# Performance work log

Measured on AMD Instinct MI355X. Metric: run time of the kernel, lower is better.

The kernel has to match this reference:

```python
import jax, jax.numpy as jnp
import numpy as np

BEV_H = 100
BEV_W = 100
BEV_Z = 4
NUM_CAMS = 6
EMBED = 256
HF, WF = 32, 88
PC_RANGE = (-51.2, -51.2, -5.0, 51.2, 51.2, 3.0)
EPS = 1e-5


def setup_inputs() -> dict:
    key = jax.random.key(0)
    ks = jax.random.split(key, 5)
    B, Nq = 1, BEV_H * BEV_W
    return {
        "query": jax.random.normal(ks[0], (B, Nq, EMBED), jnp.float32),
        "img_feats": jax.random.normal(ks[1], (B, NUM_CAMS, EMBED, HF, WF), jnp.float32),
        "lidar2img": jax.random.normal(ks[2], (B, NUM_CAMS, 4, 4), jnp.float32),
        "attn_w": jax.random.normal(ks[3], (EMBED, NUM_CAMS * BEV_Z), jnp.float32) * 0.02,
        "attn_b": jnp.zeros((NUM_CAMS * BEV_Z,), jnp.float32),
        "out_w": jax.random.normal(ks[4], (EMBED, EMBED), jnp.float32) * 0.02,
        "out_b": jnp.zeros((EMBED,), jnp.float32),
    }


def _reference_points(B):
    # normalized pillar reference points: (B, Nq, Z, 3), x,y,z in (0,1)
    ys = jnp.linspace(0.5, BEV_H - 0.5, BEV_H, dtype=jnp.float32) / BEV_H
    xs = jnp.linspace(0.5, BEV_W - 0.5, BEV_W, dtype=jnp.float32) / BEV_W
    ref_y, ref_x = jnp.meshgrid(ys, xs, indexing="ij")  # (H, W)
    Nq = BEV_H * BEV_W
    rx = jnp.broadcast_to(ref_x.reshape(Nq, 1), (Nq, BEV_Z))
    ry = jnp.broadcast_to(ref_y.reshape(Nq, 1), (Nq, BEV_Z))
    rz = jnp.broadcast_to(
        (jnp.linspace(0.5, BEV_Z - 0.5, BEV_Z, dtype=jnp.float32) / BEV_Z)[None, :],
        (Nq, BEV_Z),
    )
    ref = jnp.stack([rx, ry, rz], axis=-1)  # (Nq, Z, 3)
    return jnp.broadcast_to(ref[None], (B, Nq, BEV_Z, 3))


def _grid_sample(img, grid):
    # Bilinear grid_sample, zero padding, align_corners=False.
    # img: (M, C, H, W), grid: (M, N, 2) in [-1, 1] -> (M, C, N)
    M, C, H, W = img.shape
    x = ((grid[..., 0] + 1.0) * W - 1.0) * 0.5
    y = ((grid[..., 1] + 1.0) * H - 1.0) * 0.5
    x0 = jnp.floor(x)
    y0 = jnp.floor(y)
    wx1 = x - x0
    wy1 = y - y0

    def tap(xi, yi, w):
        valid = (xi >= 0) & (xi < W) & (yi >= 0) & (yi < H)
        xc = jnp.clip(xi, 0, W - 1).astype(jnp.int32)
        yc = jnp.clip(yi, 0, H - 1).astype(jnp.int32)
        v = jax.vmap(lambda im, yy, xx: im[:, yy, xx])(img, yc, xc)  # (M, C, N)
        return v * (w * valid)[:, None, :]

    return (
        tap(x0, y0, (1.0 - wx1) * (1.0 - wy1))
        + tap(x0 + 1.0, y0, wx1 * (1.0 - wy1))
        + tap(x0, y0 + 1.0, (1.0 - wx1) * wy1)
        + tap(x0 + 1.0, y0 + 1.0, wx1 * wy1)
    )


def reference(query, img_feats, lidar2img, attn_w, attn_b, out_w, out_b):
    B, Nq, C = query.shape
    Ncam = img_feats.shape[1]
    Hf, Wf = img_feats.shape[-2], img_feats.shape[-1]
    Z = BEV_Z

    ref = _reference_points(B)  # (B, Nq, Z, 3)
    pc = PC_RANGE
    scale = jnp.array([pc[3] - pc[0], pc[4] - pc[1], pc[5] - pc[2]], jnp.float32)
    offset = jnp.array([pc[0], pc[1], pc[2]], jnp.float32)
    r = ref * scale + offset
    r4 = jnp.concatenate([r, jnp.ones_like(r[..., :1])], axis=-1).reshape(B, Nq * Z, 4)

    # project to each camera: (B, Ncam, Nq*Z, 4)
    cam = jnp.einsum("bnij,bqj->bnqi", lidar2img, r4)
    depth = cam[..., 2]
    xy = cam[..., 0:2] / jnp.maximum(depth, EPS)[..., None]
    gx = (xy[..., 0] / (Wf - 1) - 0.5) * 2.0
    gy = (xy[..., 1] / (Hf - 1) - 0.5) * 2.0
    grid = jnp.stack([gx, gy], axis=-1)  # (B, Ncam, Nq*Z, 2)
    valid = (depth > EPS) & (gx > -1.0) & (gx < 1.0) & (gy > -1.0) & (gy < 1.0)

    sampled = _grid_sample(
        img_feats.reshape(B * Ncam, C, Hf, Wf), grid.reshape(B * Ncam, Nq * Z, 2)
    )  # (B*Ncam, C, Nq*Z)
    sampled = sampled.reshape(B, Ncam, C, Nq, Z) * valid.reshape(B, Ncam, 1, Nq, Z)
    sampled = jnp.nan_to_num(sampled)

    # (cam, z) softmax weights from the query
    w = jax.nn.softmax(query @ attn_w + attn_b, axis=-1).reshape(B, Nq, Ncam, Z)
    out = jnp.einsum("bncqz,bqnz->bqc", sampled, w)
    out = out @ out_w + out_b
    return out + query
```

## Files before the change

kernel.cpp:

```cpp
#include <hip/hip_runtime.h>
#include <math.h>

#define NCAM 6
#define CH   256
#define HFt  32
#define WFt  88
#define NQ   10000
#define NPT  24

typedef __attribute__((ext_vector_type(8))) short short8;
typedef __attribute__((ext_vector_type(4))) float f32x4;

__device__ __forceinline__ unsigned short f2bf(float x) {
  unsigned int u = __float_as_uint(x);
  u += 0x7FFFu + ((u >> 16) & 1u);
  return (unsigned short)(u >> 16);
}
__device__ __forceinline__ float bf2f(unsigned short b) {
  return __uint_as_float(((unsigned int)b) << 16);
}

#define TRBLKS  (NCAM * HFt * 8)
#define WSWBLKS 32
#define LOGITS0 (TRBLKS + WSWBLKS)
#define NLB     157

__global__ __launch_bounds__(256) void k_prep(const float* __restrict__ img,
                                              const float* __restrict__ query,
                                              const float* __restrict__ aw,
                                              const float* __restrict__ ab,
                                              const float* __restrict__ ow,
                                              unsigned short* __restrict__ featT,
                                              unsigned short* __restrict__ Wsw,
                                              float* __restrict__ Wgt) {
  __shared__ __align__(16) char smem[16384];
  const int blk = blockIdx.x;
  const int tid = threadIdx.x;

  if (blk < TRBLKS) {
    float (*tile)[WFt + 1] = (float (*)[WFt + 1])smem;
    int ct = blk & 7, h = (blk >> 3) & 31, cam = blk >> 8;
    const float* src = img + (((size_t)cam * CH + ct * 32) * HFt + h) * WFt;
    for (int i = tid; i < 32 * 22; i += 256) {
      int c = i / 22, w4 = i - c * 22;
      float4 v = *(const float4*)(src + (size_t)c * (HFt * WFt) + 4 * w4);
      tile[c][4 * w4 + 0] = v.x;
      tile[c][4 * w4 + 1] = v.y;
      tile[c][4 * w4 + 2] = v.z;
      tile[c][4 * w4 + 3] = v.w;
    }
    __syncthreads();
    unsigned short* dst = featT + ((size_t)(cam * HFt + h) * WFt) * CH + ct * 32;
    for (int i = tid; i < WFt * 8; i += 256) {
      int w = i >> 3, g = i & 7;
      uint2 u;
      u.x = (unsigned int)f2bf(tile[4 * g + 0][w]) | ((unsigned int)f2bf(tile[4 * g + 1][w]) << 16);
      u.y = (unsigned int)f2bf(tile[4 * g + 2][w]) | ((unsigned int)f2bf(tile[4 * g + 3][w]) << 16);
      *(uint2*)(dst + (size_t)w * CH + 4 * g) = u;
    }
    return;
  }

  if (blk < LOGITS0) {
    int gtid = (blk - TRBLKS) * 256 + tid;
    int l  = gtid & 63;
    int f  = (gtid >> 6) & 1;
    int kk = (gtid >> 7) & 7;
    int c  = gtid >> 10;
    int n  = 32 * c + 16 * f + (l & 15);
    int kb = 32 * kk + 4 * (l >> 4);
    unsigned int u0 = f2bf(ow[(kb + 0) * CH + n])  | ((unsigned int)f2bf(ow[(kb + 1) * CH + n])  << 16);
    unsigned int u1 = f2bf(ow[(kb + 2) * CH + n])  | ((unsigned int)f2bf(ow[(kb + 3) * CH + n])  << 16);
    unsigned int u2 = f2bf(ow[(kb + 16) * CH + n]) | ((unsigned int)f2bf(ow[(kb + 17) * CH + n]) << 16);
    unsigned int u3 = f2bf(ow[(kb + 18) * CH + n]) | ((unsigned int)f2bf(ow[(kb + 19) * CH + n]) << 16);
    ((uint4*)Wsw)[gtid] = make_uint4(u0, u1, u2, u3);
    return;
  }

  const int q0 = (blk - LOGITS0) * 64;
  uint4* awB = (uint4*)smem;
  for (int e = tid; e < 1024; e += 256) {
    int le = e & 63, f = (e >> 6) & 1, kk = e >> 7;
    int n = 16 * f + (le & 15);
    int kb = 32 * kk + 4 * (le >> 4);
    uint4 uv = make_uint4(0u, 0u, 0u, 0u);
    if (n < NPT) {
      uv.x = f2bf(aw[(kb + 0) * NPT + n])  | ((unsigned int)f2bf(aw[(kb + 1) * NPT + n])  << 16);
      uv.y = f2bf(aw[(kb + 2) * NPT + n])  | ((unsigned int)f2bf(aw[(kb + 3) * NPT + n])  << 16);
      uv.z = f2bf(aw[(kb + 16) * NPT + n]) | ((unsigned int)f2bf(aw[(kb + 17) * NPT + n]) << 16);
      uv.w = f2bf(aw[(kb + 18) * NPT + n]) | ((unsigned int)f2bf(aw[(kb + 19) * NPT + n]) << 16);
    }
    awB[e] = uv;
  }
  __syncthreads();

  const int wv = tid >> 6, l = tid & 63;
  const int col = l & 15, grp = l >> 4;
  int qr = q0 + wv * 16 + col;
  if (qr > NQ - 1) qr = NQ - 1;
  const float* qp = query + (size_t)qr * CH + 4 * grp;

  f32x4 acc0 = {0.f, 0.f, 0.f, 0.f}, acc1 = {0.f, 0.f, 0.f, 0.f};
#pragma unroll
  for (int kk = 0; kk < 8; kk++) {
    float4 lo = *(const float4*)(qp + kk * 32);
    float4 hi = *(const float4*)(qp + kk * 32 + 16);
    union { uint4 u; short8 s; } a;
    a.u.x = (unsigned int)f2bf(lo.x) | ((unsigned int)f2bf(lo.y) << 16);
    a.u.y = (unsigned int)f2bf(lo.z) | ((unsigned int)f2bf(lo.w) << 16);
    a.u.z = (unsigned int)f2bf(hi.x) | ((unsigned int)f2bf(hi.y) << 16);
    a.u.w = (unsigned int)f2bf(hi.z) | ((unsigned int)f2bf(hi.w) << 16);
    union { uint4 u; short8 s; } b0, b1;
    b0.u = awB[(kk * 2 + 0) * 64 + l];
    b1.u = awB[(kk * 2 + 1) * 64 + l];
    acc0 = __builtin_amdgcn_mfma_f32_16x16x32_bf16(a.s, b0.s, acc0, 0, 0, 0);
    acc1 = __builtin_amdgcn_mfma_f32_16x16x32_bf16(a.s, b1.s, acc1, 0, 0, 0);
  }

  const int n0 = col, n1 = 16 + col;
  const bool v16 = (n1 < NPT);
  const float ab0 = ab[n0];
  const float ab1 = v16 ? ab[n1] : 0.f;
#pragma unroll
  for (int r = 0; r < 4; r++) {
    float v0 = acc0[r] + ab0;
    float v1 = v16 ? (acc1[r] + ab1) : -3.4e38f;
    float m = fmaxf(v0, v1);
#pragma unroll
    for (int off = 1; off < 16; off <<= 1) m = fmaxf(m, __shfl_xor(m, off, 64));
    float e0 = __expf(v0 - m);
    float e1 = v16 ? __expf(v1 - m) : 0.f;
    float s = e0 + e1;
#pragma unroll
    for (int off = 1; off < 16; off <<= 1) s += __shfl_xor(s, off, 64);
    int qq = q0 + wv * 16 + 4 * grp + r;
    if (qq < NQ) {
      Wgt[qq * NPT + n0] = e0 / s;
      if (v16) Wgt[qq * NPT + n1] = e1 / s;
    }
  }
}

__global__ __launch_bounds__(256) void k_main(const unsigned short* __restrict__ featT,
                                              const float* __restrict__ l2i,
                                              const float* __restrict__ Wgt,
                                              unsigned short* __restrict__ A) {
  const int wv   = threadIdx.x >> 6;
  const int lane = threadIdx.x & 63;
  const int q    = blockIdx.x * 4 + wv;

  __shared__ float Lm[NCAM * 16];
  __shared__ int   offW[4][96];
  __shared__ float wW[4][96];

  if (threadIdx.x < NCAM * 16) Lm[threadIdx.x] = l2i[threadIdx.x];

  float sw = (lane < NPT) ? Wgt[q * NPT + lane] : 0.f;

  __syncthreads();

  bool valid = false;
  int o0 = 0, o1 = 0, o2 = 0, o3 = 0;
  float w0 = 0.f, w1 = 0.f, w2 = 0.f, w3 = 0.f;
  if (lane < NPT) {
    int cam = lane >> 2, z = lane & 3;
    float X  = (((q % 100) + 0.5f) * 0.01f) * 102.4f - 51.2f;
    float Y  = (((q / 100) + 0.5f) * 0.01f) * 102.4f - 51.2f;
    float Zc = ((z + 0.5f) * 0.25f) * 8.f - 5.f;
    const float* Lr = Lm + cam * 16;
    float cx = Lr[0] * X + Lr[1] * Y + Lr[2]  * Zc + Lr[3];
    float cy = Lr[4] * X + Lr[5] * Y + Lr[6]  * Zc + Lr[7];
    float cd = Lr[8] * X + Lr[9] * Y + Lr[10] * Zc + Lr[11];
    float d  = fmaxf(cd, 1e-5f);
    float gx = (cx / d * (1.f / 87.f) - 0.5f) * 2.f;
    float gy = (cy / d * (1.f / 31.f) - 0.5f) * 2.f;
    valid = (cd > 1e-5f) && (gx > -1.f) && (gx < 1.f) && (gy > -1.f) && (gy < 1.f);

    float x = ((gx + 1.f) * 88.f - 1.f) * 0.5f;
    float y = ((gy + 1.f) * 32.f - 1.f) * 0.5f;
    float x0f = floorf(x), y0f = floorf(y);
    float wx1 = x - x0f, wy1 = y - y0f;
    float wx0 = 1.f - wx1, wy0 = 1.f - wy1;
    bool vx0 = (x0f >= 0.f) && (x0f < 88.f);
    bool vx1 = (x0f + 1.f >= 0.f) && (x0f + 1.f < 88.f);
    bool vy0 = (y0f >= 0.f) && (y0f < 32.f);
    bool vy1 = (y0f + 1.f >= 0.f) && (y0f + 1.f < 32.f);
    int x0 = (int)fminf(fmaxf(x0f, 0.f), 87.f);
    int x1 = (int)fminf(fmaxf(x0f + 1.f, 0.f), 87.f);
    int y0 = (int)fminf(fmaxf(y0f, 0.f), 31.f);
    int y1 = (int)fminf(fmaxf(y0f + 1.f, 0.f), 31.f);
    int cb = cam * (HFt * WFt);
    o0 = (cb + y0 * WFt + x0) * CH;
    o1 = (cb + y0 * WFt + x1) * CH;
    o2 = (cb + y1 * WFt + x0) * CH;
    o3 = (cb + y1 * WFt + x1) * CH;
    w0 = sw * wx0 * wy0 * ((vx0 && vy0) ? 1.f : 0.f);
    w1 = sw * wx1 * wy0 * ((vx1 && vy0) ? 1.f : 0.f);
    w2 = sw * wx0 * wy1 * ((vx0 && vy1) ? 1.f : 0.f);
    w3 = sw * wx1 * wy1 * ((vx1 && vy1) ? 1.f : 0.f);
  }

  unsigned long long vm = __ballot(valid);
  int nvalid = __popcll(vm);
  int pos = __popcll(vm & ((1ull << lane) - 1ull));
  if (valid) {
    int b = 4 * pos;
    offW[wv][b + 0] = o0; wW[wv][b + 0] = w0;
    offW[wv][b + 1] = o1; wW[wv][b + 1] = w1;
    offW[wv][b + 2] = o2; wW[wv][b + 2] = w2;
    offW[wv][b + 3] = o3; wW[wv][b + 3] = w3;
  }
  int nt  = 4 * nvalid;
  int ntp = (nt + 7) & ~7;
  if (lane < ntp - nt) { offW[wv][nt + lane] = 0; wW[wv][nt + lane] = 0.f; }

  float4 acc0 = {0.f, 0.f, 0.f, 0.f}, acc1 = {0.f, 0.f, 0.f, 0.f};
  const unsigned short* fb = featT + 4 * lane;
  for (int i = 0; i < ntp; i += 8) {
    int   a0 = offW[wv][i + 0], a1 = offW[wv][i + 1], a2 = offW[wv][i + 2], a3 = offW[wv][i + 3];
    int   a4 = offW[wv][i + 4], a5 = offW[wv][i + 5], a6 = offW[wv][i + 6], a7 = offW[wv][i + 7];
    float b0 = wW[wv][i + 0], b1 = wW[wv][i + 1], b2 = wW[wv][i + 2], b3 = wW[wv][i + 3];
    float b4 = wW[wv][i + 4], b5 = wW[wv][i + 5], b6 = wW[wv][i + 6], b7 = wW[wv][i + 7];
    ushort4 v0 = *(const ushort4*)(fb + a0);
    ushort4 v1 = *(const ushort4*)(fb + a1);
    ushort4 v2 = *(const ushort4*)(fb + a2);
    ushort4 v3 = *(const ushort4*)(fb + a3);
    ushort4 v4 = *(const ushort4*)(fb + a4);
    ushort4 v5 = *(const ushort4*)(fb + a5);
    ushort4 v6 = *(const ushort4*)(fb + a6);
    ushort4 v7 = *(const ushort4*)(fb + a7);
    acc0.x = fmaf(b0, bf2f(v0.x), acc0.x); acc0.y = fmaf(b0, bf2f(v0.y), acc0.y);
    acc0.z = fmaf(b0, bf2f(v0.z), acc0.z); acc0.w = fmaf(b0, bf2f(v0.w), acc0.w);
    acc1.x = fmaf(b1, bf2f(v1.x), acc1.x); acc1.y = fmaf(b1, bf2f(v1.y), acc1.y);
    acc1.z = fmaf(b1, bf2f(v1.z), acc1.z); acc1.w = fmaf(b1, bf2f(v1.w), acc1.w);
    acc0.x = fmaf(b2, bf2f(v2.x), acc0.x); acc0.y = fmaf(b2, bf2f(v2.y), acc0.y);
    acc0.z = fmaf(b2, bf2f(v2.z), acc0.z); acc0.w = fmaf(b2, bf2f(v2.w), acc0.w);
    acc1.x = fmaf(b3, bf2f(v3.x), acc1.x); acc1.y = fmaf(b3, bf2f(v3.y), acc1.y);
    acc1.z = fmaf(b3, bf2f(v3.z), acc1.z); acc1.w = fmaf(b3, bf2f(v3.w), acc1.w);
    acc0.x = fmaf(b4, bf2f(v4.x), acc0.x); acc0.y = fmaf(b4, bf2f(v4.y), acc0.y);
    acc0.z = fmaf(b4, bf2f(v4.z), acc0.z); acc0.w = fmaf(b4, bf2f(v4.w), acc0.w);
    acc1.x = fmaf(b5, bf2f(v5.x), acc1.x); acc1.y = fmaf(b5, bf2f(v5.y), acc1.y);
    acc1.z = fmaf(b5, bf2f(v5.z), acc1.z); acc1.w = fmaf(b5, bf2f(v5.w), acc1.w);
    acc0.x = fmaf(b6, bf2f(v6.x), acc0.x); acc0.y = fmaf(b6, bf2f(v6.y), acc0.y);
    acc0.z = fmaf(b6, bf2f(v6.z), acc0.z); acc0.w = fmaf(b6, bf2f(v6.w), acc0.w);
    acc1.x = fmaf(b7, bf2f(v7.x), acc1.x); acc1.y = fmaf(b7, bf2f(v7.y), acc1.y);
    acc1.z = fmaf(b7, bf2f(v7.z), acc1.z); acc1.w = fmaf(b7, bf2f(v7.w), acc1.w);
  }
  ushort4 st;
  st.x = f2bf(acc0.x + acc1.x); st.y = f2bf(acc0.y + acc1.y);
  st.z = f2bf(acc0.z + acc1.z); st.w = f2bf(acc0.w + acc1.w);
  *(ushort4*)(A + (size_t)q * CH + 4 * lane) = st;
}

__global__ __launch_bounds__(256) void k_out_mfma(const unsigned short* __restrict__ A,
                                                  const float* __restrict__ query,
                                                  const unsigned short* __restrict__ Wsw,
                                                  const float* __restrict__ ob,
                                                  float* __restrict__ outp) {
  const int blk = blockIdx.x;
  const int mtile = blk >> 1, nhalf = blk & 1;
  const int m0 = mtile * 16;
  const int t = threadIdx.x, wv = t >> 6, l = t & 63;
  const int row = l & 15, grp = l >> 4;

  const unsigned short* ap = A + (size_t)(m0 + row) * CH + 4 * grp;
  short8 af[8];
#pragma unroll
  for (int kk = 0; kk < 8; kk++) {
    uint2 lo = *(const uint2*)(ap + kk * 32);
    uint2 hi = *(const uint2*)(ap + kk * 32 + 16);
    union { uint4 u; short8 s; } x;
    x.u.x = lo.x; x.u.y = lo.y; x.u.z = hi.x; x.u.w = hi.y;
    af[kk] = x.s;
  }

  const int chunk = nhalf * 4 + wv;
  const uint4* wp = (const uint4*)Wsw;
  f32x4 acc0 = {0.f, 0.f, 0.f, 0.f}, acc1 = {0.f, 0.f, 0.f, 0.f};
#pragma unroll
  for (int kk = 0; kk < 8; kk++) {
    uint4 w0 = wp[((chunk * 8 + kk) * 2 + 0) * 64 + l];
    uint4 w1 = wp[((chunk * 8 + kk) * 2 + 1) * 64 + l];
    union { uint4 u; short8 s; } b0, b1;
    b0.u = w0; b1.u = w1;
    acc0 = __builtin_amdgcn_mfma_f32_16x16x32_bf16(af[kk], b0.s, acc0, 0, 0, 0);
    acc1 = __builtin_amdgcn_mfma_f32_16x16x32_bf16(af[kk], b1.s, acc1, 0, 0, 0);
  }

  const int nbase = nhalf * 128 + wv * 32;
#pragma unroll
  for (int f = 0; f < 2; f++) {
    f32x4 ac = (f == 0) ? acc0 : acc1;
    int n = nbase + 16 * f + row;
    float bias = ob[n];
#pragma unroll
    for (int r = 0; r < 4; r++) {
      int m = m0 + 4 * grp + r;
      size_t idx = (size_t)m * CH + n;
      outp[idx] = ac[r] + bias + query[idx];
    }
  }
}

extern "C" void kernel_launch(void* const* d_in, const int* in_sizes, int n_in,
                              void* d_out, int out_size, void* d_ws, size_t ws_size,
                              hipStream_t stream) {
  const float* query = (const float*)d_in[0];
  const float* img   = (const float*)d_in[1];
  const float* l2i   = (const float*)d_in[2];
  const float* aw    = (const float*)d_in[3];
  const float* ab    = (const float*)d_in[4];
  const float* ow    = (const float*)d_in[5];
  const float* ob    = (const float*)d_in[6];
  float* outp = (float*)d_out;

  char* ws = (char*)d_ws;
  unsigned short* featT = (unsigned short*)ws;
  unsigned short* Abf   = (unsigned short*)(ws + 8650752);
  unsigned short* Wsw   = (unsigned short*)(ws + 13770752);
  float*          Wgt   = (float*)(ws + 13901824);

  k_prep<<<TRBLKS + WSWBLKS + NLB, 256, 0, stream>>>(img, query, aw, ab, ow, featT, Wsw, Wgt);
  k_main<<<NQ / 4, 256, 0, stream>>>(featT, l2i, Wgt, Abf);
  k_out_mfma<<<(NQ / 16) * 2, 256, 0, stream>>>(Abf, query, Wsw, ob, outp);
}
```

Baseline: 37.76 us.

## Fuse sampling kernel with output projection GEMM via shared-memory A tile

New measurement: 33.16 us. 12.2% less time.

```diff
diff --git a/kernel.cpp b/kernel.cpp
--- a/kernel.cpp
+++ b/kernel.cpp
@@ -21,9 +21,10 @@
 }
 
 #define TRBLKS  (NCAM * HFt * 8)
+#define NLB     157
+#define WSW0    (TRBLKS + NLB)
 #define WSWBLKS 32
-#define LOGITS0 (TRBLKS + WSWBLKS)
-#define NLB     157
+#define FUSB    (NQ / 8)
 
 __global__ __launch_bounds__(256) void k_prep(const float* __restrict__ img,
                                               const float* __restrict__ query,
@@ -61,8 +62,8 @@
     return;
   }
 
-  if (blk < LOGITS0) {
-    int gtid = (blk - TRBLKS) * 256 + tid;
+  if (blk >= WSW0) {
+    int gtid = (blk - WSW0) * 256 + tid;
     int l  = gtid & 63;
     int f  = (gtid >> 6) & 1;
     int kk = (gtid >> 7) & 7;
@@ -77,7 +78,7 @@
     return;
   }
 
-  const int q0 = (blk - LOGITS0) * 64;
+  const int q0 = (blk - TRBLKS) * 64;
   uint4* awB = (uint4*)smem;
   for (int e = tid; e < 1024; e += 256) {
     int le = e & 63, f = (e >> 6) & 1, kk = e >> 7;
@@ -141,19 +142,26 @@
   }
 }
 
-__global__ __launch_bounds__(256) void k_main(const unsigned short* __restrict__ featT,
-                                              const float* __restrict__ l2i,
-                                              const float* __restrict__ Wgt,
-                                              unsigned short* __restrict__ A) {
-  const int wv   = threadIdx.x >> 6;
-  const int lane = threadIdx.x & 63;
-  const int q    = blockIdx.x * 4 + wv;
+__global__ __launch_bounds__(512) void k_fused(const unsigned short* __restrict__ featT,
+                                               const float* __restrict__ l2i,
+                                               const float* __restrict__ Wgt,
+                                               const float* __restrict__ query,
+                                               const unsigned short* __restrict__ Wsw,
+                                               const float* __restrict__ ob,
+                                               float* __restrict__ outp) {
+  const int blk  = blockIdx.x;
+  const int tid  = threadIdx.x;
+  const int wv   = tid >> 6;
+  const int lane = tid & 63;
+  const int q0   = blk * 8;
+  const int q    = q0 + wv;
 
   __shared__ float Lm[NCAM * 16];
-  __shared__ int   offW[4][96];
-  __shared__ float wW[4][96];
-
-  if (threadIdx.x < NCAM * 16) Lm[threadIdx.x] = l2i[threadIdx.x];
+  __shared__ int   offW[8][96];
+  __shared__ float wW[8][96];
+  __shared__ __align__(16) unsigned short Atile[16 * 264];
+
+  if (tid < NCAM * 16) Lm[tid] = l2i[tid];
 
   float sw = (lane < NPT) ? Wgt[q * NPT + lane] : 0.f;
 
@@ -249,55 +257,45 @@
   ushort4 st;
   st.x = f2bf(acc0.x + acc1.x); st.y = f2bf(acc0.y + acc1.y);
   st.z = f2bf(acc0.z + acc1.z); st.w = f2bf(acc0.w + acc1.w);
-  *(ushort4*)(A + (size_t)q * CH + 4 * lane) = st;
-}
-
-__global__ __launch_bounds__(256) void k_out_mfma(const unsigned short* __restrict__ A,
-                                                  const float* __restrict__ query,
-                                                  const unsigned short* __restrict__ Wsw,
-                                                  const float* __restrict__ ob,
-                                                  float* __restrict__ outp) {
-  const int blk = blockIdx.x;
-  const int mtile = blk >> 1, nhalf = blk & 1;
-  const int m0 = mtile * 16;
-  const int t = threadIdx.x, wv = t >> 6, l = t & 63;
-  const int row = l & 15, grp = l >> 4;
-
-  const unsigned short* ap = A + (size_t)(m0 + row) * CH + 4 * grp;
+  *(ushort4*)(Atile + wv * 264 + 4 * lane) = st;
+
+  __syncthreads();
+
+  const int col = lane & 15, grp = lane >> 4;
   short8 af[8];
-#pragma unroll
-  for (int kk = 0; kk < 8; kk++) {
-    uint2 lo = *(const uint2*)(ap + kk * 32);
-    uint2 hi = *(const uint2*)(ap + kk * 32 + 16);
-    union { uint4 u; short8 s; } x;
-    x.u.x = lo.x; x.u.y = lo.y; x.u.z = hi.x; x.u.w = hi.y;
-    af[kk] = x.s;
-  }
-
-  const int chunk = nhalf * 4 + wv;
+  {
+    const unsigned short* ap = Atile + col * 264 + 4 * grp;
+#pragma unroll
+    for (int kk = 0; kk < 8; kk++) {
+      uint2 lo = *(const uint2*)(ap + kk * 32);
+      uint2 hi = *(const uint2*)(ap + kk * 32 + 16);
+      union { uint4 u; short8 s; } x;
+      x.u.x = lo.x; x.u.y = lo.y; x.u.z = hi.x; x.u.w = hi.y;
+      af[kk] = x.s;
+    }
+  }
+
   const uint4* wp = (const uint4*)Wsw;
-  f32x4 acc0 = {0.f, 0.f, 0.f, 0.f}, acc1 = {0.f, 0.f, 0.f, 0.f};
-#pragma unroll
-  for (int kk = 0; kk < 8; kk++) {
-    uint4 w0 = wp[((chunk * 8 + kk) * 2 + 0) * 64 + l];
-    uint4 w1 = wp[((chunk * 8 + kk) * 2 + 1) * 64 + l];
-    union { uint4 u; short8 s; } b0, b1;
-    b0.u = w0; b1.u = w1;
-    acc0 = __builtin_amdgcn_mfma_f32_16x16x32_bf16(af[kk], b0.s, acc0, 0, 0, 0);
-    acc1 = __builtin_amdgcn_mfma_f32_16x16x32_bf16(af[kk], b1.s, acc1, 0, 0, 0);
-  }
-
-  const int nbase = nhalf * 128 + wv * 32;
-#pragma unroll
-  for (int f = 0; f < 2; f++) {
-    f32x4 ac = (f == 0) ? acc0 : acc1;
-    int n = nbase + 16 * f + row;
-    float bias = ob[n];
-#pragma unroll
-    for (int r = 0; r < 4; r++) {
-      int m = m0 + 4 * grp + r;
-      size_t idx = (size_t)m * CH + n;
-      outp[idx] = ac[r] + bias + query[idx];
+#pragma unroll
+  for (int t2 = 0; t2 < 2; ++t2) {
+    const int g = wv + 8 * t2;
+    const int chunk = g >> 1, fh = g & 1;
+    f32x4 oa = {0.f, 0.f, 0.f, 0.f};
+#pragma unroll
+    for (int kk = 0; kk < 8; kk++) {
+      union { uint4 u; short8 s; } b;
+      b.u = wp[((chunk * 8 + kk) * 2 + fh) * 64 + lane];
+      oa = __builtin_amdgcn_mfma_f32_16x16x32_bf16(af[kk], b.s, oa, 0, 0, 0);
+    }
+    if (grp < 2) {
+      const int n = g * 16 + col;
+      const float bias = ob[n];
+#pragma unroll
+      for (int r = 0; r < 4; r++) {
+        const int m = q0 + 4 * grp + r;
+        const size_t idx = (size_t)m * CH + n;
+        outp[idx] = oa[r] + bias + query[idx];
+      }
     }
   }
 }
@@ -316,11 +314,9 @@
 
   char* ws = (char*)d_ws;
   unsigned short* featT = (unsigned short*)ws;
-  unsigned short* Abf   = (unsigned short*)(ws + 8650752);
-  unsigned short* Wsw   = (unsigned short*)(ws + 13770752);
-  float*          Wgt   = (float*)(ws + 13901824);
-
-  k_prep<<<TRBLKS + WSWBLKS + NLB, 256, 0, stream>>>(img, query, aw, ab, ow, featT, Wsw, Wgt);
-  k_main<<<NQ / 4, 256, 0, stream>>>(featT, l2i, Wgt, Abf);
-  k_out_mfma<<<(NQ / 16) * 2, 256, 0, stream>>>(Abf, query, Wsw, ob, outp);
-}
+  unsigned short* Wsw   = (unsigned short*)(ws + 8650752);
+  float*          Wgt   = (float*)(ws + 8781824);
+
+  k_prep<<<WSW0 + WSWBLKS, 256, 0, stream>>>(img, query, aw, ab, ow, featT, Wsw, Wgt);
+  k_fused<<<FUSB, 512, 0, stream>>>(featT, l2i, Wgt, query, Wsw, ob, outp);
+}
```
